# Performance work log

Measured on AMD Instinct MI355X. Metric: run time of the kernel, lower is better.

Reference implementation:

```python
import jax, jax.numpy as jnp
import numpy as np

IN_FEATURES = 4096
OUT_FEATURES = 4096
GROUP_SIZE = 128


def setup_inputs() -> dict:
    key = jax.random.key(0)
    k1, k2, k3 = jax.random.split(key, 3)
    x = jax.random.normal(k1, (4, 2048, IN_FEATURES), dtype=jnp.float32)
    # ternary codes in {-1, 0, 1}
    ternary = jax.random.randint(k2, (OUT_FEATURES, IN_FEATURES), -1, 2, dtype=jnp.int32).astype(jnp.int8)
    n_groups = OUT_FEATURES * IN_FEATURES // GROUP_SIZE
    # per-group positive scales (beta = mean |w| per group in the original init)
    scales = jax.random.uniform(k3, (n_groups,), dtype=jnp.float32, minval=0.01, maxval=0.2)
    return {"x": x, "ternary": ternary, "scales": scales}


def reference(x, ternary, scales):
    # Reconstruct fp32 weight: each contiguous group of GROUP_SIZE weights
    # (row-major over [out, in]) shares one scale.
    w = ternary.astype(jnp.float32).reshape(-1, GROUP_SIZE) * scales[:, None]
    w = w.reshape(OUT_FEATURES, IN_FEATURES)
    # F.linear: y = x @ W^T
    return jnp.einsum('bsi,oi->bso', x, w)
```

## Files before the change

kernel.cpp:

```cpp
#include <hip/hip_runtime.h>


typedef int intx4 __attribute__((ext_vector_type(4)));

constexpr int K  = 4096;
constexpr int N  = 4096;
constexpr int NG = 32;

__device__ __forceinline__ void gload_lds16(const void* gsrc, void* ldst) {
  const __attribute__((address_space(1))) unsigned* g =
      reinterpret_cast<const __attribute__((address_space(1))) unsigned*>(
          reinterpret_cast<uintptr_t>(gsrc));
  __attribute__((address_space(3))) unsigned* l =
      reinterpret_cast<__attribute__((address_space(3))) unsigned*>(
          reinterpret_cast<uintptr_t>(ldst));
  __builtin_amdgcn_global_load_lds(g, l, 16, 0, 0);
}

__global__ __launch_bounds__(256) void quant_x_kernel(const float* __restrict__ x,
                                                      char* __restrict__ q,
                                                      float* __restrict__ sx) {
  const int row = blockIdx.x;
  const int tid = threadIdx.x;
  const float4* xr = reinterpret_cast<const float4*>(x + (long)row * K);
  float4 v[4];
  float am = 0.f;
#pragma unroll
  for (int j = 0; j < 4; ++j) {
    v[j] = xr[tid * 4 + j];
    am = fmaxf(am, fmaxf(fmaxf(fabsf(v[j].x), fabsf(v[j].y)),
                         fmaxf(fabsf(v[j].z), fabsf(v[j].w))));
  }
#pragma unroll
  for (int off = 32; off > 0; off >>= 1)
    am = fmaxf(am, __shfl_xor(am, off));
  __shared__ float wmax[4];
  if ((tid & 63) == 0) wmax[tid >> 6] = am;
  __syncthreads();
  am = fmaxf(fmaxf(wmax[0], wmax[1]), fmaxf(wmax[2], wmax[3]));
  const float inv = am > 0.f ? 127.f / am : 0.f;
  int t[16];
#pragma unroll
  for (int j = 0; j < 4; ++j) {
    t[j * 4 + 0] = (int)rintf(v[j].x * inv);
    t[j * 4 + 1] = (int)rintf(v[j].y * inv);
    t[j * 4 + 2] = (int)rintf(v[j].z * inv);
    t[j * 4 + 3] = (int)rintf(v[j].w * inv);
  }
  int4 o;
  o.x = (t[0] & 255) | ((t[1] & 255) << 8) | ((t[2] & 255) << 16) | ((t[3] & 255) << 24);
  o.y = (t[4] & 255) | ((t[5] & 255) << 8) | ((t[6] & 255) << 16) | ((t[7] & 255) << 24);
  o.z = (t[8] & 255) | ((t[9] & 255) << 8) | ((t[10] & 255) << 16) | ((t[11] & 255) << 24);
  o.w = (t[12] & 255) | ((t[13] & 255) << 8) | ((t[14] & 255) << 16) | ((t[15] & 255) << 24);
  reinterpret_cast<int4*>(q + (long)row * K)[tid] = o;
  if (tid == 0) sx[row] = am * (1.f / 127.f);
}

__global__ __launch_bounds__(256) void pack_w_kernel(const int* __restrict__ w,
                                                     const float* __restrict__ s,
                                                     char* __restrict__ o,
                                                     float* __restrict__ sw) {
  const int row = blockIdx.x;
  const int tid = threadIdx.x;
  __shared__ float Ssh;
  if (tid < 64) {
    float v = (tid < NG) ? s[(long)row * NG + tid] : 0.f;
#pragma unroll
    for (int off = 32; off > 0; off >>= 1)
      v = fmaxf(v, __shfl_xor(v, off));
    if (tid == 0) {
      Ssh = v;
      sw[row] = v * (1.f / 127.f);
    }
  }
  __syncthreads();
  const float S = Ssh;
  const int g = tid >> 3;
  const int m = (int)rintf(127.f * s[(long)row * NG + g] / S);
  const int4* src = reinterpret_cast<const int4*>(w + (long)row * K + tid * 16);
  int4 a = src[0], b = src[1], c = src[2], d = src[3];
  int4 r;
  r.x = ((a.x * m) & 255) | (((a.y * m) & 255) << 8) |
        (((a.z * m) & 255) << 16) | (((a.w * m) & 255) << 24);
  r.y = ((b.x * m) & 255) | (((b.y * m) & 255) << 8) |
        (((b.z * m) & 255) << 16) | (((b.w * m) & 255) << 24);
  r.z = ((c.x * m) & 255) | (((c.y * m) & 255) << 8) |
        (((c.z * m) & 255) << 16) | (((c.w * m) & 255) << 24);
  r.w = ((d.x * m) & 255) | (((d.y * m) & 255) << 8) |
        (((d.z * m) & 255) << 16) | (((d.w * m) & 255) << 24);
  reinterpret_cast<int4*>(o + (long)row * K)[tid] = r;
}


__device__ __forceinline__ intx4 ldfrag(const char* region, int row, int slot) {
  return *reinterpret_cast<const intx4*>(region + row * 128 +
                                         (slot ^ ((row & 7) << 4)));
}

__device__ __forceinline__ void stage_half(const char* gmat, char* lregion,
                                           int k0, int h, int wid, int l) {
#pragma unroll
  for (int load = 0; load < 2; ++load) {
    const int row = h * 128 + load * 64 + wid * 8 + (l >> 3);
    const int col = ((l & 7) ^ ((l >> 3) & 7)) << 4;
    const char* g = gmat + (long)row * K + k0 + col;
    char* ldst = lregion + h * 16384 + load * 8192 + wid * 1024;
    gload_lds16(g, ldst);
  }
}

template <int Q>
__device__ __forceinline__ void loadApair(intx4 (&afr)[2][2], const char* ar,
                                          int wr, int rlo, int kq) {
#pragma unroll
  for (int mi = 0; mi < 2; ++mi)
#pragma unroll
    for (int ks = 0; ks < 2; ++ks)
      afr[mi][ks] = ldfrag(ar, wr * 128 + (2 * Q + mi) * 16 + rlo,
                           ks * 64 + kq * 16);
}

__device__ __forceinline__ void loadBall(intx4 (&bfr)[4][2], const char* br,
                                         int wc, int rlo, int kq) {
#pragma unroll
  for (int nt = 0; nt < 4; ++nt)
#pragma unroll
    for (int ks = 0; ks < 2; ++ks)
      bfr[nt][ks] = ldfrag(br, wc * 64 + nt * 16 + rlo, ks * 64 + kq * 16);
}

template <int Q>
__device__ __forceinline__ void mmaQ(intx4 (&acc)[8][4], intx4 (&afr)[2][2],
                                     intx4 (&bfr)[4][2]) {
  __builtin_amdgcn_s_setprio(1);
#pragma unroll
  for (int mi = 0; mi < 2; ++mi)
#pragma unroll
    for (int nt = 0; nt < 4; ++nt) {
      acc[2 * Q + mi][nt] = __builtin_amdgcn_mfma_i32_16x16x64_i8(
          afr[mi][0], bfr[nt][0], acc[2 * Q + mi][nt], 0, 0, 0);
      acc[2 * Q + mi][nt] = __builtin_amdgcn_mfma_i32_16x16x64_i8(
          afr[mi][1], bfr[nt][1], acc[2 * Q + mi][nt], 0, 0, 0);
    }
  __builtin_amdgcn_s_setprio(0);
}

#define FENCE asm volatile("" ::: "memory")
#define BAR                       \
  do {                            \
    __builtin_amdgcn_s_barrier(); \
    FENCE;                        \
  } while (0)
#define LGKM0  asm volatile("s_waitcnt lgkmcnt(0)" ::: "memory")
#define VMCNT6 asm volatile("s_waitcnt vmcnt(6)" ::: "memory")
#define VMCNT0 asm volatile("s_waitcnt vmcnt(0)" ::: "memory")

__global__ __launch_bounds__(512) void gemm8p(
    const char* __restrict__ A, const char* __restrict__ B,
    const float* __restrict__ SW, const float* __restrict__ SX,
    float* __restrict__ C) {
  __shared__ char lds[131072];
  const int tid = threadIdx.x;
  const int wid = tid >> 6, l = tid & 63;
  const int wr = wid >> 2, wc = wid & 3;
  const int rlo = l & 15, kq = l >> 4;

  const int wg = blockIdx.x;
  const int swz = (wg & 7) * 64 + (wg >> 3);
  const long brow = (long)(swz >> 4) * 256;
  const long bcol = (long)(swz & 15) * 256;

  const char* gA = A + brow * K;
  const char* gB = B + bcol * K;
  char* a0 = lds;
  char* b0 = lds + 32768;
  char* a1 = lds + 65536;
  char* b1 = lds + 98304;

  stage_half(gB, b0, 0, 0, wid, l);
  stage_half(gB, b0, 0, 1, wid, l);
  stage_half(gA, a0, 0, 0, wid, l);
  stage_half(gA, a0, 0, 1, wid, l);
  stage_half(gB, b1, 128, 0, wid, l);
  stage_half(gB, b1, 128, 1, wid, l);
  stage_half(gA, a1, 128, 0, wid, l);
  VMCNT6;
  BAR;

  intx4 acc[8][4] = {};
  intx4 afr[2][2], bfr[4][2];

#pragma unroll 1
  for (int it = 0; it < 15; ++it) {
    const int kt1 = (2 * it + 1) * 128, kt2 = kt1 + 128, kt3 = kt2 + 128;
    loadBall(bfr, b0, wc, rlo, kq);
    loadApair<0>(afr, a0, wr, rlo, kq);
    stage_half(gA, a1, kt1, 1, wid, l);
    BAR; LGKM0;
    mmaQ<0>(acc, afr, bfr);
    BAR;
    loadApair<1>(afr, a0, wr, rlo, kq);
    stage_half(gB, b0, kt2, 0, wid, l);
    BAR; LGKM0;
    mmaQ<1>(acc, afr, bfr);
    BAR;
    loadApair<2>(afr, a0, wr, rlo, kq);
    stage_half(gB, b0, kt2, 1, wid, l);
    BAR; LGKM0;
    mmaQ<2>(acc, afr, bfr);
    BAR;
    loadApair<3>(afr, a0, wr, rlo, kq);
    stage_half(gA, a0, kt2, 0, wid, l);
    BAR; LGKM0;
    mmaQ<3>(acc, afr, bfr);
    VMCNT6;
    BAR;
    loadBall(bfr, b1, wc, rlo, kq);
    loadApair<0>(afr, a1, wr, rlo, kq);
    stage_half(gA, a0, kt2, 1, wid, l);
    BAR; LGKM0;
    mmaQ<0>(acc, afr, bfr);
    BAR;
    loadApair<1>(afr, a1, wr, rlo, kq);
    stage_half(gB, b1, kt3, 0, wid, l);
    BAR; LGKM0;
    mmaQ<1>(acc, afr, bfr);
    BAR;
    loadApair<2>(afr, a1, wr, rlo, kq);
    stage_half(gB, b1, kt3, 1, wid, l);
    BAR; LGKM0;
    mmaQ<2>(acc, afr, bfr);
    BAR;
    loadApair<3>(afr, a1, wr, rlo, kq);
    stage_half(gA, a1, kt3, 0, wid, l);
    BAR; LGKM0;
    mmaQ<3>(acc, afr, bfr);
    VMCNT6;
    BAR;
  }

  loadBall(bfr, b0, wc, rlo, kq);
  loadApair<0>(afr, a0, wr, rlo, kq);
  stage_half(gA, a1, 31 * 128, 1, wid, l);
  BAR; LGKM0;
  mmaQ<0>(acc, afr, bfr);
  BAR;
  loadApair<1>(afr, a0, wr, rlo, kq);
  BAR; LGKM0;
  mmaQ<1>(acc, afr, bfr);
  BAR;
  loadApair<2>(afr, a0, wr, rlo, kq);
  BAR; LGKM0;
  mmaQ<2>(acc, afr, bfr);
  BAR;
  loadApair<3>(afr, a0, wr, rlo, kq);
  BAR; LGKM0;
  mmaQ<3>(acc, afr, bfr);
  VMCNT0;
  BAR;
  loadBall(bfr, b1, wc, rlo, kq);
  loadApair<0>(afr, a1, wr, rlo, kq);
  LGKM0;
  mmaQ<0>(acc, afr, bfr);
  loadApair<1>(afr, a1, wr, rlo, kq);
  mmaQ<1>(acc, afr, bfr);
  loadApair<2>(afr, a1, wr, rlo, kq);
  mmaQ<2>(acc, afr, bfr);
  loadApair<3>(afr, a1, wr, rlo, kq);
  mmaQ<3>(acc, afr, bfr);

  const long crow0 = brow + wr * 128 + kq * 4;
  const long ccol = bcol + wc * 64 + rlo;
  float swn[4];
#pragma unroll
  for (int nt = 0; nt < 4; ++nt) swn[nt] = SW[ccol + nt * 16];
#pragma unroll
  for (int mi = 0; mi < 8; ++mi) {
    const float4 sx4 = *reinterpret_cast<const float4*>(SX + crow0 + mi * 16);
    const float sxr[4] = {sx4.x, sx4.y, sx4.z, sx4.w};
#pragma unroll
    for (int nt = 0; nt < 4; ++nt) {
      float* cp = C + (crow0 + mi * 16) * (long)N + ccol + nt * 16;
#pragma unroll
      for (int r = 0; r < 4; ++r)
        cp[r * N] = (float)acc[mi][nt][r] * sxr[r] * swn[nt];
    }
  }
}

__global__ void fallback_kernel(const float* __restrict__ x,
                                const int* __restrict__ t,
                                const float* __restrict__ s,
                                float* __restrict__ y) {
  int n = blockIdx.x * 256 + threadIdx.x;
  int m = blockIdx.y;
  const int* tr = t + (long)n * K;
  const float* xr = x + (long)m * K;
  float acc = 0.f;
  for (int g = 0; g < K / 128; ++g) {
    float scv = s[n * (K / 128) + g];
    float part = 0.f;
#pragma unroll 4
    for (int k = g * 128; k < g * 128 + 128; ++k)
      part += xr[k] * (float)tr[k];
    acc += part * scv;
  }
  y[(long)m * N + n] = acc;
}

extern "C" void kernel_launch(void* const* d_in, const int* in_sizes, int n_in,
                              void* d_out, int out_size, void* d_ws,
                              size_t ws_size, hipStream_t stream) {
  const float* x = (const float*)d_in[0];
  const int* tern = (const int*)d_in[1];
  const float* scales = (const float*)d_in[2];
  float* out = (float*)d_out;

  const long M = (long)in_sizes[0] / K;
  const size_t offW = (size_t)M * K;
  const size_t offSW = offW + (size_t)N * K;
  const size_t offSX = offSW + (size_t)N * 4;
  const size_t need = offSX + (size_t)M * 4;

  if (ws_size >= need && (M % 256) == 0) {
    char* Aq = (char*)d_ws;
    char* Wq = (char*)d_ws + offW;
    float* SW = (float*)((char*)d_ws + offSW);
    float* SX = (float*)((char*)d_ws + offSX);

    quant_x_kernel<<<(unsigned)M, 256, 0, stream>>>(x, Aq, SX);
    pack_w_kernel<<<(unsigned)N, 256, 0, stream>>>(tern, scales, Wq, SW);

    const unsigned nblk = (unsigned)((M / 256) * (N / 256));
    gemm8p<<<nblk, 512, 0, stream>>>(Aq, Wq, SW, SX, out);
  } else {
    dim3 grid(N / 256, (unsigned)M);
    fallback_kernel<<<grid, 256, 0, stream>>>(x, tern, scales, out);
  }
}
```

Before: 180.1 us.

## Replace pipelined 256x256 int8 GEMM with simple single-buffered 128x128 tile kernel

Swaps the hand-pipelined 512-thread 256x256 tile kernel, which used double-buffered 128KB LDS and interleaved staging with MFMA, for a 256-thread 128x128 tile kernel. The new kernel stages each K-slice into 32KB LDS, waits for all loads, then computes, targeting three blocks per CU for occupancy-based latency hiding. It gives up the explicit global-load/compute overlap and halves reuse per tile, which raises global and L2 traffic. The block swizzle and the grid size are adjusted to match the new tile.

```diff
diff --git a/kernel.cpp b/kernel.cpp
--- a/kernel.cpp
+++ b/kernel.cpp
@@ -97,52 +97,13 @@
                                          (slot ^ ((row & 7) << 4)));
 }
 
-__device__ __forceinline__ void stage_half(const char* gmat, char* lregion,
-                                           int k0, int h, int wid, int l) {
-#pragma unroll
-  for (int load = 0; load < 2; ++load) {
-    const int row = h * 128 + load * 64 + wid * 8 + (l >> 3);
-    const int col = ((l & 7) ^ ((l >> 3) & 7)) << 4;
-    const char* g = gmat + (long)row * K + k0 + col;
-    char* ldst = lregion + h * 16384 + load * 8192 + wid * 1024;
-    gload_lds16(g, ldst);
-  }
-}
-
-template <int Q>
-__device__ __forceinline__ void loadApair(intx4 (&afr)[2][2], const char* ar,
-                                          int wr, int rlo, int kq) {
-#pragma unroll
-  for (int mi = 0; mi < 2; ++mi)
-#pragma unroll
-    for (int ks = 0; ks < 2; ++ks)
-      afr[mi][ks] = ldfrag(ar, wr * 128 + (2 * Q + mi) * 16 + rlo,
-                           ks * 64 + kq * 16);
-}
-
-__device__ __forceinline__ void loadBall(intx4 (&bfr)[4][2], const char* br,
-                                         int wc, int rlo, int kq) {
-#pragma unroll
-  for (int nt = 0; nt < 4; ++nt)
-#pragma unroll
-    for (int ks = 0; ks < 2; ++ks)
-      bfr[nt][ks] = ldfrag(br, wc * 64 + nt * 16 + rlo, ks * 64 + kq * 16);
-}
-
-template <int Q>
-__device__ __forceinline__ void mmaQ(intx4 (&acc)[8][4], intx4 (&afr)[2][2],
-                                     intx4 (&bfr)[4][2]) {
-  __builtin_amdgcn_s_setprio(1);
-#pragma unroll
-  for (int mi = 0; mi < 2; ++mi)
-#pragma unroll
-    for (int nt = 0; nt < 4; ++nt) {
-      acc[2 * Q + mi][nt] = __builtin_amdgcn_mfma_i32_16x16x64_i8(
-          afr[mi][0], bfr[nt][0], acc[2 * Q + mi][nt], 0, 0, 0);
-      acc[2 * Q + mi][nt] = __builtin_amdgcn_mfma_i32_16x16x64_i8(
-          afr[mi][1], bfr[nt][1], acc[2 * Q + mi][nt], 0, 0, 0);
-    }
-  __builtin_amdgcn_s_setprio(0);
+__device__ __forceinline__ void stage_round(const char* gmat, char* lregion,
+                                            int k0, int rnd, int wid, int l) {
+  const int row = rnd * 32 + wid * 8 + (l >> 3);
+  const int col = ((l & 7) ^ ((l >> 3) & 7)) << 4;
+  const char* g = gmat + (long)row * K + k0 + col;
+  char* ldst = lregion + rnd * 4096 + wid * 1024;
+  gload_lds16(g, ldst);
 }
 
 #define FENCE asm volatile("" ::: "memory")
@@ -151,131 +112,66 @@
     __builtin_amdgcn_s_barrier(); \
     FENCE;                        \
   } while (0)
-#define LGKM0  asm volatile("s_waitcnt lgkmcnt(0)" ::: "memory")
-#define VMCNT6 asm volatile("s_waitcnt vmcnt(6)" ::: "memory")
 #define VMCNT0 asm volatile("s_waitcnt vmcnt(0)" ::: "memory")
 
-__global__ __launch_bounds__(512) void gemm8p(
+__global__ __launch_bounds__(256, 3) void gemm_i8(
     const char* __restrict__ A, const char* __restrict__ B,
     const float* __restrict__ SW, const float* __restrict__ SX,
     float* __restrict__ C) {
-  __shared__ char lds[131072];
+  __shared__ char As[16384];
+  __shared__ char Bs[16384];
   const int tid = threadIdx.x;
   const int wid = tid >> 6, l = tid & 63;
-  const int wr = wid >> 2, wc = wid & 3;
+  const int wr = wid >> 1, wc = wid & 1;
   const int rlo = l & 15, kq = l >> 4;
 
   const int wg = blockIdx.x;
-  const int swz = (wg & 7) * 64 + (wg >> 3);
-  const long brow = (long)(swz >> 4) * 256;
-  const long bcol = (long)(swz & 15) * 256;
+  const int swz = (wg & 7) * 256 + (wg >> 3);
+  const long brow = (long)(swz >> 5) * 128;
+  const long bcol = (long)(swz & 31) * 128;
 
   const char* gA = A + brow * K;
   const char* gB = B + bcol * K;
-  char* a0 = lds;
-  char* b0 = lds + 32768;
-  char* a1 = lds + 65536;
-  char* b1 = lds + 98304;
-
-  stage_half(gB, b0, 0, 0, wid, l);
-  stage_half(gB, b0, 0, 1, wid, l);
-  stage_half(gA, a0, 0, 0, wid, l);
-  stage_half(gA, a0, 0, 1, wid, l);
-  stage_half(gB, b1, 128, 0, wid, l);
-  stage_half(gB, b1, 128, 1, wid, l);
-  stage_half(gA, a1, 128, 0, wid, l);
-  VMCNT6;
-  BAR;
-
-  intx4 acc[8][4] = {};
-  intx4 afr[2][2], bfr[4][2];
+
+  intx4 acc[4][4] = {};
 
 #pragma unroll 1
-  for (int it = 0; it < 15; ++it) {
-    const int kt1 = (2 * it + 1) * 128, kt2 = kt1 + 128, kt3 = kt2 + 128;
-    loadBall(bfr, b0, wc, rlo, kq);
-    loadApair<0>(afr, a0, wr, rlo, kq);
-    stage_half(gA, a1, kt1, 1, wid, l);
-    BAR; LGKM0;
-    mmaQ<0>(acc, afr, bfr);
+  for (int t = 0; t < 32; ++t) {
+    const int k0 = t << 7;
+#pragma unroll
+    for (int r = 0; r < 4; ++r) stage_round(gA, As, k0, r, wid, l);
+#pragma unroll
+    for (int r = 0; r < 4; ++r) stage_round(gB, Bs, k0, r, wid, l);
+    VMCNT0;
     BAR;
-    loadApair<1>(afr, a0, wr, rlo, kq);
-    stage_half(gB, b0, kt2, 0, wid, l);
-    BAR; LGKM0;
-    mmaQ<1>(acc, afr, bfr);
+#pragma unroll
+    for (int ks = 0; ks < 2; ++ks) {
+      intx4 af[4], bf[4];
+#pragma unroll
+      for (int mi = 0; mi < 4; ++mi)
+        af[mi] = ldfrag(As, wr * 64 + mi * 16 + rlo, ks * 64 + kq * 16);
+#pragma unroll
+      for (int nt = 0; nt < 4; ++nt)
+        bf[nt] = ldfrag(Bs, wc * 64 + nt * 16 + rlo, ks * 64 + kq * 16);
+      __builtin_amdgcn_s_setprio(1);
+#pragma unroll
+      for (int mi = 0; mi < 4; ++mi)
+#pragma unroll
+        for (int nt = 0; nt < 4; ++nt)
+          acc[mi][nt] = __builtin_amdgcn_mfma_i32_16x16x64_i8(
+              af[mi], bf[nt], acc[mi][nt], 0, 0, 0);
+      __builtin_amdgcn_s_setprio(0);
+    }
     BAR;
-    loadApair<2>(afr, a0, wr, rlo, kq);
-    stage_half(gB, b0, kt2, 1, wid, l);
-    BAR; LGKM0;
-    mmaQ<2>(acc, afr, bfr);
-    BAR;
-    loadApair<3>(afr, a0, wr, rlo, kq);
-    stage_half(gA, a0, kt2, 0, wid, l);
-    BAR; LGKM0;
-    mmaQ<3>(acc, afr, bfr);
-    VMCNT6;
-    BAR;
-    loadBall(bfr, b1, wc, rlo, kq);
-    loadApair<0>(afr, a1, wr, rlo, kq);
-    stage_half(gA, a0, kt2, 1, wid, l);
-    BAR; LGKM0;
-    mmaQ<0>(acc, afr, bfr);
-    BAR;
-    loadApair<1>(afr, a1, wr, rlo, kq);
-    stage_half(gB, b1, kt3, 0, wid, l);
-    BAR; LGKM0;
-    mmaQ<1>(acc, afr, bfr);
-    BAR;
-    loadApair<2>(afr, a1, wr, rlo, kq);
-    stage_half(gB, b1, kt3, 1, wid, l);
-    BAR; LGKM0;
-    mmaQ<2>(acc, afr, bfr);
-    BAR;
-    loadApair<3>(afr, a1, wr, rlo, kq);
-    stage_half(gA, a1, kt3, 0, wid, l);
-    BAR; LGKM0;
-    mmaQ<3>(acc, afr, bfr);
-    VMCNT6;
-    BAR;
-  }
-
-  loadBall(bfr, b0, wc, rlo, kq);
-  loadApair<0>(afr, a0, wr, rlo, kq);
-  stage_half(gA, a1, 31 * 128, 1, wid, l);
-  BAR; LGKM0;
-  mmaQ<0>(acc, afr, bfr);
-  BAR;
-  loadApair<1>(afr, a0, wr, rlo, kq);
-  BAR; LGKM0;
-  mmaQ<1>(acc, afr, bfr);
-  BAR;
-  loadApair<2>(afr, a0, wr, rlo, kq);
-  BAR; LGKM0;
-  mmaQ<2>(acc, afr, bfr);
-  BAR;
-  loadApair<3>(afr, a0, wr, rlo, kq);
-  BAR; LGKM0;
-  mmaQ<3>(acc, afr, bfr);
-  VMCNT0;
-  BAR;
-  loadBall(bfr, b1, wc, rlo, kq);
-  loadApair<0>(afr, a1, wr, rlo, kq);
-  LGKM0;
-  mmaQ<0>(acc, afr, bfr);
-  loadApair<1>(afr, a1, wr, rlo, kq);
-  mmaQ<1>(acc, afr, bfr);
-  loadApair<2>(afr, a1, wr, rlo, kq);
-  mmaQ<2>(acc, afr, bfr);
-  loadApair<3>(afr, a1, wr, rlo, kq);
-  mmaQ<3>(acc, afr, bfr);
-
-  const long crow0 = brow + wr * 128 + kq * 4;
+  }
+
+  const long crow0 = brow + wr * 64 + kq * 4;
   const long ccol = bcol + wc * 64 + rlo;
   float swn[4];
 #pragma unroll
   for (int nt = 0; nt < 4; ++nt) swn[nt] = SW[ccol + nt * 16];
 #pragma unroll
-  for (int mi = 0; mi < 8; ++mi) {
+  for (int mi = 0; mi < 4; ++mi) {
     const float4 sx4 = *reinterpret_cast<const float4*>(SX + crow0 + mi * 16);
     const float sxr[4] = {sx4.x, sx4.y, sx4.z, sx4.w};
 #pragma unroll
@@ -322,7 +218,7 @@
   const size_t offSX = offSW + (size_t)N * 4;
   const size_t need = offSX + (size_t)M * 4;
 
-  if (ws_size >= need && (M % 256) == 0) {
+  if (ws_size >= need && (M % 128) == 0) {
     char* Aq = (char*)d_ws;
     char* Wq = (char*)d_ws + offW;
     float* SW = (float*)((char*)d_ws + offSW);
@@ -331,8 +227,8 @@
     quant_x_kernel<<<(unsigned)M, 256, 0, stream>>>(x, Aq, SX);
     pack_w_kernel<<<(unsigned)N, 256, 0, stream>>>(tern, scales, Wq, SW);
 
-    const unsigned nblk = (unsigned)((M / 256) * (N / 256));
-    gemm8p<<<nblk, 512, 0, stream>>>(Aq, Wq, SW, SX, out);
+    const unsigned nblk = (unsigned)((M / 128) * (N / 128));
+    gemm_i8<<<nblk, 256, 0, stream>>>(Aq, Wq, SW, SX, out);
   } else {
     dim3 grid(N / 256, (unsigned)M);
     fallback_kernel<<<grid, 256, 0, stream>>>(x, tern, scales, out);
```

Measured after the change: 207.7 us. 1.15x slower.
